# Kernel optimization log

Measured on AMD Instinct MI355X. Metric: run time of the kernel, lower is better.

The kernel has to match this reference:

```python
import jax, jax.numpy as jnp
import numpy as np

B = 32768
NUM_CLASS = 1000
FEATURE_DIM = 512


def setup_inputs() -> dict:
    key = jax.random.key(0)
    k1, k2, k3 = jax.random.split(key, 3)
    features = jax.random.normal(k1, (B, FEATURE_DIM), dtype=jnp.float32)
    labels = jax.random.randint(k2, (B,), 0, NUM_CLASS, dtype=jnp.int32)
    center = jax.random.normal(k3, (NUM_CLASS, FEATURE_DIM), dtype=jnp.float32)
    return {"features": features, "labels": labels, "center": center}


def reference(features, labels, center):
    C = center.shape[0]
    # ---- intra loss: per-row euclidean distance to own-class center ----
    # (equivalent to gathering dist_mat[i, labels[i]] from cdist(features, center, p=2))
    diff = features - center[labels]                      # [B, D]
    dist = jnp.sqrt(jnp.sum(diff * diff, axis=-1))        # [B]
    dist = jnp.clip(dist, 1e-12, 1e12)
    intra_loss = dist.mean()

    # ---- inter loss ----
    # torch: center.scatter_add(0, labels_rep, features) -> center_param + per-class sum
    sums = jax.ops.segment_sum(features, labels, num_segments=C)          # [C, D]
    # counts: scatter_add with index [B,1] only uses first column of ones -> class counts
    counts = jax.ops.segment_sum(jnp.ones((features.shape[0],), features.dtype),
                                 labels, num_segments=C)                  # [C]
    cen = (center + sums) / jnp.clip(counts, 1.0, None)[:, None]          # [C, D]
    # source bug: loop keeps only the LAST combination (C-2, C-1)
    d_last = jnp.sqrt(jnp.sum((cen[C - 2] - cen[C - 1]) ** 2))
    inter_loss = (2.0 / d_last) * (1.0 / (C * (C - 1)))
    return (intra_loss, inter_loss)
```

## Files before the change

kernel.cpp:

```cpp
#include <hip/hip_runtime.h>

#define B_ROWS   32768
#define NUM_CLS  1000
#define FEAT     512

#define BLOCKS          2048
#define THREADS         256
#define WAVES_PER_BLOCK 4
#define ROWS_PER_WAVE   4

typedef float f32x4 __attribute__((ext_vector_type(4)));

#define WS_CNT0   1
#define WS_CNT1   2
#define WS_SUM0   64
#define WS_SUM1   (64 + 512)
#define WS_PART   (64 + 1024)
#define WS_ZERO_FLOATS (64 + 1024)

__global__ __launch_bounds__(THREADS) void loss_pass1(
    const float* __restrict__ features,
    const int*   __restrict__ labels,
    const float* __restrict__ center,
    float*       __restrict__ ws)
{
    const int wave = threadIdx.x >> 6;
    const int lane = threadIdx.x & 63;
    const int wid  = blockIdx.x * WAVES_PER_BLOCK + wave;
    const int base_row = wid * ROWS_PER_WAVE;

    const int mylab = labels[base_row + (lane & 3)];

    float p[ROWS_PER_WAVE];

    #pragma unroll
    for (int r = 0; r < ROWS_PER_WAVE; ++r) {
        const int row = base_row + r;
        const int lab = __shfl(mylab, r);

        const f32x4* frow = (const f32x4*)(features + (size_t)row * FEAT);
        const f32x4* crow = (const f32x4*)(center   + (size_t)lab * FEAT);

        f32x4 f0 = frow[lane];
        f32x4 f1 = frow[lane + 64];
        f32x4 c0 = crow[lane];
        f32x4 c1 = crow[lane + 64];

        f32x4 d0 = f0 - c0;
        f32x4 d1 = f1 - c1;

        p[r] = d0.x*d0.x + d0.y*d0.y + d0.z*d0.z + d0.w*d0.w
             + d1.x*d1.x + d1.y*d1.y + d1.z*d1.z + d1.w*d1.w;

        if (lab >= NUM_CLS - 2) {
            float* sums = ws + (lab == NUM_CLS - 2 ? WS_SUM0 : WS_SUM1);
            const int base = lane * 4;
            atomicAdd(&sums[base + 0],   f0.x);
            atomicAdd(&sums[base + 1],   f0.y);
            atomicAdd(&sums[base + 2],   f0.z);
            atomicAdd(&sums[base + 3],   f0.w);
            atomicAdd(&sums[base + 256], f1.x);
            atomicAdd(&sums[base + 257], f1.y);
            atomicAdd(&sums[base + 258], f1.z);
            atomicAdd(&sums[base + 259], f1.w);
            if (lane == 0)
                atomicAdd(&ws[lab == NUM_CLS - 2 ? WS_CNT0 : WS_CNT1], 1.0f);
        }
    }

    const bool b0 = lane & 1, b1 = lane & 2;

    float q[2];
    #pragma unroll
    for (int i = 0; i < 2; ++i) {
        float send = b0 ? p[i]     : p[2 + i];
        float keep = b0 ? p[2 + i] : p[i];
        q[i] = keep + __shfl_xor(send, 1);
    }
    {
        float send = b1 ? q[0] : q[1];
        float keep = b1 ? q[1] : q[0];
        float u = keep + __shfl_xor(send, 2);
        u += __shfl_xor(u, 4);
        u += __shfl_xor(u, 8);
        u += __shfl_xor(u, 16);
        u += __shfl_xor(u, 32);
        float dist = sqrtf(u);
        dist = fminf(fmaxf(dist, 1e-12f), 1e12f);
        dist += __shfl_xor(dist, 1);
        dist += __shfl_xor(dist, 2);
        p[0] = dist;
    }

    __shared__ float s[WAVES_PER_BLOCK];
    if (lane == 0) s[wave] = p[0];
    __syncthreads();
    if (threadIdx.x == 0)
        ws[WS_PART + blockIdx.x] = s[0] + s[1] + s[2] + s[3];
}

__global__ __launch_bounds__(256) void loss_pass2(
    const float* __restrict__ center,
    const float* __restrict__ ws,
    float*       __restrict__ out)
{
    const int t = threadIdx.x;
    const float cnt0 = fmaxf(ws[WS_CNT0], 1.0f);
    const float cnt1 = fmaxf(ws[WS_CNT1], 1.0f);

    float p_inter = 0.0f;
    #pragma unroll
    for (int k = 0; k < 2; ++k) {
        const int d = t * 2 + k;
        float a = (center[(size_t)(NUM_CLS - 2) * FEAT + d] + ws[WS_SUM0 + d]) / cnt0;
        float b = (center[(size_t)(NUM_CLS - 1) * FEAT + d] + ws[WS_SUM1 + d]) / cnt1;
        float df = a - b;
        p_inter += df * df;
    }

    float p_intra = 0.0f;
    #pragma unroll
    for (int k = 0; k < 8; ++k)
        p_intra += ws[WS_PART + t + k * 256];

    #pragma unroll
    for (int off = 32; off; off >>= 1) {
        p_inter += __shfl_xor(p_inter, off);
        p_intra += __shfl_xor(p_intra, off);
    }

    __shared__ float si[4], sa[4];
    if ((t & 63) == 0) { si[t >> 6] = p_inter; sa[t >> 6] = p_intra; }
    __syncthreads();

    if (t == 0) {
        float d_last = sqrtf(si[0] + si[1] + si[2] + si[3]);
        out[0] = (sa[0] + sa[1] + sa[2] + sa[3]) * (1.0f / (float)B_ROWS);
        out[1] = (2.0f / d_last) * (1.0f / ((float)NUM_CLS * (float)(NUM_CLS - 1)));
    }
}

extern "C" void kernel_launch(void* const* d_in, const int* in_sizes, int n_in,
                              void* d_out, int out_size, void* d_ws, size_t ws_size,
                              hipStream_t stream) {
    const float* features = (const float*)d_in[0];
    const int*   labels   = (const int*)d_in[1];
    const float* center   = (const float*)d_in[2];
    float* out = (float*)d_out;
    float* ws  = (float*)d_ws;

    (void)hipMemsetAsync(ws, 0, WS_ZERO_FLOATS * sizeof(float), stream);

    loss_pass1<<<BLOCKS, THREADS, 0, stream>>>(features, labels, center, ws);
    loss_pass2<<<1, 256, 0, stream>>>(center, ws, out);
}
```

Before: 25.58 us.

## Move last-two-class sums into pass2 via label scan, drop memset and global atomics

Pass1 no longer does global atomic accumulation for the two last classes. Pass2 now scans all labels, builds a shared list of matching rows, and sums those rows with shared-memory atomics. The workspace memset is no longer needed, and pass1 issues all feature loads before the center loads. The risk is that the list is capped at CAP=192 rows, so any matches past that are silently dropped. Pass2 also becomes a serial single-block scan over 32K labels.

```diff
diff --git a/kernel.cpp b/kernel.cpp
--- a/kernel.cpp
+++ b/kernel.cpp
@@ -9,14 +9,10 @@
 #define WAVES_PER_BLOCK 4
 #define ROWS_PER_WAVE   4
 
+#define CAP 192
+
 typedef float f32x4 __attribute__((ext_vector_type(4)));
 
-#define WS_CNT0   1
-#define WS_CNT1   2
-#define WS_SUM0   64
-#define WS_SUM1   (64 + 512)
-#define WS_PART   (64 + 1024)
-#define WS_ZERO_FLOATS (64 + 1024)
 
 __global__ __launch_bounds__(THREADS) void loss_pass1(
     const float* __restrict__ features,
@@ -31,41 +27,28 @@
 
     const int mylab = labels[base_row + (lane & 3)];
 
-    float p[ROWS_PER_WAVE];
-
+    f32x4 f[8], c[8];
     #pragma unroll
     for (int r = 0; r < ROWS_PER_WAVE; ++r) {
-        const int row = base_row + r;
+        const f32x4* frow = (const f32x4*)(features + (size_t)(base_row + r) * FEAT);
+        f[2*r]     = frow[lane];
+        f[2*r + 1] = frow[lane + 64];
+    }
+    #pragma unroll
+    for (int r = 0; r < ROWS_PER_WAVE; ++r) {
         const int lab = __shfl(mylab, r);
+        const f32x4* crow = (const f32x4*)(center + (size_t)lab * FEAT);
+        c[2*r]     = crow[lane];
+        c[2*r + 1] = crow[lane + 64];
+    }
 
-        const f32x4* frow = (const f32x4*)(features + (size_t)row * FEAT);
-        const f32x4* crow = (const f32x4*)(center   + (size_t)lab * FEAT);
-
-        f32x4 f0 = frow[lane];
-        f32x4 f1 = frow[lane + 64];
-        f32x4 c0 = crow[lane];
-        f32x4 c1 = crow[lane + 64];
-
-        f32x4 d0 = f0 - c0;
-        f32x4 d1 = f1 - c1;
-
+    float p[ROWS_PER_WAVE];
+    #pragma unroll
+    for (int r = 0; r < ROWS_PER_WAVE; ++r) {
+        f32x4 d0 = f[2*r]     - c[2*r];
+        f32x4 d1 = f[2*r + 1] - c[2*r + 1];
         p[r] = d0.x*d0.x + d0.y*d0.y + d0.z*d0.z + d0.w*d0.w
              + d1.x*d1.x + d1.y*d1.y + d1.z*d1.z + d1.w*d1.w;
-
-        if (lab >= NUM_CLS - 2) {
-            float* sums = ws + (lab == NUM_CLS - 2 ? WS_SUM0 : WS_SUM1);
-            const int base = lane * 4;
-            atomicAdd(&sums[base + 0],   f0.x);
-            atomicAdd(&sums[base + 1],   f0.y);
-            atomicAdd(&sums[base + 2],   f0.z);
-            atomicAdd(&sums[base + 3],   f0.w);
-            atomicAdd(&sums[base + 256], f1.x);
-            atomicAdd(&sums[base + 257], f1.y);
-            atomicAdd(&sums[base + 258], f1.z);
-            atomicAdd(&sums[base + 259], f1.w);
-            if (lane == 0)
-                atomicAdd(&ws[lab == NUM_CLS - 2 ? WS_CNT0 : WS_CNT1], 1.0f);
-        }
     }
 
     const bool b0 = lane & 1, b1 = lane & 2;
@@ -77,6 +60,7 @@
         float keep = b0 ? p[2 + i] : p[i];
         q[i] = keep + __shfl_xor(send, 1);
     }
+    float acc;
     {
         float send = b1 ? q[0] : q[1];
         float keep = b1 ? q[1] : q[0];
@@ -89,39 +73,85 @@
         dist = fminf(fmaxf(dist, 1e-12f), 1e12f);
         dist += __shfl_xor(dist, 1);
         dist += __shfl_xor(dist, 2);
-        p[0] = dist;
+        acc = dist;
     }
 
     __shared__ float s[WAVES_PER_BLOCK];
-    if (lane == 0) s[wave] = p[0];
+    if (lane == 0) s[wave] = acc;
     __syncthreads();
     if (threadIdx.x == 0)
-        ws[WS_PART + blockIdx.x] = s[0] + s[1] + s[2] + s[3];
+        ws[blockIdx.x] = s[0] + s[1] + s[2] + s[3];
 }
 
-__global__ __launch_bounds__(256) void loss_pass2(
+__global__ __launch_bounds__(1024) void loss_pass2(
+    const float* __restrict__ features,
+    const int*   __restrict__ labels,
     const float* __restrict__ center,
     const float* __restrict__ ws,
     float*       __restrict__ out)
 {
-    const int t = threadIdx.x;
-    const float cnt0 = fmaxf(ws[WS_CNT0], 1.0f);
-    const float cnt1 = fmaxf(ws[WS_CNT1], 1.0f);
+    const int t    = threadIdx.x;
+    const int wave = t >> 6;
+    const int lane = t & 63;
+
+    __shared__ float sum0[FEAT], sum1[FEAT];
+    __shared__ int   list[CAP];
+    __shared__ char  clsv[CAP];
+    __shared__ int   nmatch, cnt0_s, cnt1_s;
+
+    if (t < FEAT) { sum0[t] = 0.0f; sum1[t] = 0.0f; }
+    if (t == 0)   { nmatch = 0; cnt0_s = 0; cnt1_s = 0; }
+    __syncthreads();
+
+    const int4* lab4 = (const int4*)labels;
+    #pragma unroll
+    for (int k = 0; k < 8; ++k) {
+        const int j = t + k * 1024;
+        int4 L = lab4[j];
+        const int row0 = 4 * j;
+        if (L.x >= NUM_CLS - 2) { int i = atomicAdd(&nmatch, 1); if (i < CAP) { list[i] = row0;     clsv[i] = (char)(L.x - (NUM_CLS - 2)); } }
+        if (L.y >= NUM_CLS - 2) { int i = atomicAdd(&nmatch, 1); if (i < CAP) { list[i] = row0 + 1; clsv[i] = (char)(L.y - (NUM_CLS - 2)); } }
+        if (L.z >= NUM_CLS - 2) { int i = atomicAdd(&nmatch, 1); if (i < CAP) { list[i] = row0 + 2; clsv[i] = (char)(L.z - (NUM_CLS - 2)); } }
+        if (L.w >= NUM_CLS - 2) { int i = atomicAdd(&nmatch, 1); if (i < CAP) { list[i] = row0 + 3; clsv[i] = (char)(L.w - (NUM_CLS - 2)); } }
+    }
+    __syncthreads();
+
+    const int nm = min(nmatch, CAP);
+
+    if (t < nm) {
+        if (clsv[t] == 0) atomicAdd(&cnt0_s, 1);
+        else              atomicAdd(&cnt1_s, 1);
+    }
+
+    for (int i = wave; i < nm; i += 16) {
+        const int row = list[i];
+        float* dst = clsv[i] ? sum1 : sum0;
+        const f32x4* frow = (const f32x4*)(features + (size_t)row * FEAT);
+        f32x4 f0 = frow[lane];
+        f32x4 f1 = frow[lane + 64];
+        const int b = lane * 4;
+        atomicAdd(&dst[b + 0],   f0.x);
+        atomicAdd(&dst[b + 1],   f0.y);
+        atomicAdd(&dst[b + 2],   f0.z);
+        atomicAdd(&dst[b + 3],   f0.w);
+        atomicAdd(&dst[b + 256], f1.x);
+        atomicAdd(&dst[b + 257], f1.y);
+        atomicAdd(&dst[b + 258], f1.z);
+        atomicAdd(&dst[b + 259], f1.w);
+    }
+    __syncthreads();
 
     float p_inter = 0.0f;
-    #pragma unroll
-    for (int k = 0; k < 2; ++k) {
-        const int d = t * 2 + k;
-        float a = (center[(size_t)(NUM_CLS - 2) * FEAT + d] + ws[WS_SUM0 + d]) / cnt0;
-        float b = (center[(size_t)(NUM_CLS - 1) * FEAT + d] + ws[WS_SUM1 + d]) / cnt1;
+    if (t < FEAT) {
+        const float cnt0 = fmaxf((float)cnt0_s, 1.0f);
+        const float cnt1 = fmaxf((float)cnt1_s, 1.0f);
+        float a = (center[(size_t)(NUM_CLS - 2) * FEAT + t] + sum0[t]) / cnt0;
+        float b = (center[(size_t)(NUM_CLS - 1) * FEAT + t] + sum1[t]) / cnt1;
         float df = a - b;
-        p_inter += df * df;
+        p_inter = df * df;
     }
 
-    float p_intra = 0.0f;
-    #pragma unroll
-    for (int k = 0; k < 8; ++k)
-        p_intra += ws[WS_PART + t + k * 256];
+    float p_intra = ws[t] + ws[t + 1024];
 
     #pragma unroll
     for (int off = 32; off; off >>= 1) {
@@ -129,13 +159,16 @@
         p_intra += __shfl_xor(p_intra, off);
     }
 
-    __shared__ float si[4], sa[4];
-    if ((t & 63) == 0) { si[t >> 6] = p_inter; sa[t >> 6] = p_intra; }
+    __shared__ float si[16], sa[16];
+    if (lane == 0) { si[wave] = p_inter; sa[wave] = p_intra; }
     __syncthreads();
 
     if (t == 0) {
-        float d_last = sqrtf(si[0] + si[1] + si[2] + si[3]);
-        out[0] = (sa[0] + sa[1] + sa[2] + sa[3]) * (1.0f / (float)B_ROWS);
+        float s_inter = 0.0f, s_intra = 0.0f;
+        #pragma unroll
+        for (int i = 0; i < 16; ++i) { s_inter += si[i]; s_intra += sa[i]; }
+        float d_last = sqrtf(s_inter);
+        out[0] = s_intra * (1.0f / (float)B_ROWS);
         out[1] = (2.0f / d_last) * (1.0f / ((float)NUM_CLS * (float)(NUM_CLS - 1)));
     }
 }
@@ -149,8 +182,6 @@
     float* out = (float*)d_out;
     float* ws  = (float*)d_ws;
 
-    (void)hipMemsetAsync(ws, 0, WS_ZERO_FLOATS * sizeof(float), stream);
-
     loss_pass1<<<BLOCKS, THREADS, 0, stream>>>(features, labels, center, ws);
-    loss_pass2<<<1, 256, 0, stream>>>(center, ws, out);
+    loss_pass2<<<1, 1024, 0, stream>>>(features, labels, center, ws, out);
 }
```

Measured after the change: 69.85 us. +173.1%, slower.
